# Optimization experiments

Hardware: AMD Instinct MI355X
Metric: run time of the kernel (lower is better)

## Reference

```python
import jax, jax.numpy as jnp
import numpy as np

IN_DIM = 512
OUT_DIM = 512


def setup_inputs() -> dict:
    key = jax.random.key(0)
    ks = jax.random.split(key, 7)
    B, S = 4, 2048
    scale = 1.0 / np.sqrt(IN_DIM)
    X = jax.random.normal(ks[0], (B, S, IN_DIM), dtype=jnp.float32)
    Wq = jax.random.normal(ks[1], (IN_DIM, OUT_DIM), dtype=jnp.float32) * scale
    Wk = jax.random.normal(ks[2], (IN_DIM, OUT_DIM), dtype=jnp.float32) * scale
    Wv = jax.random.normal(ks[3], (IN_DIM, OUT_DIM), dtype=jnp.float32) * scale
    bq = jnp.zeros((OUT_DIM,), dtype=jnp.float32)
    bk = jnp.zeros((OUT_DIM,), dtype=jnp.float32)
    bv = jnp.zeros((OUT_DIM,), dtype=jnp.float32)
    return {"X": X, "Wq": Wq, "bq": bq, "Wk": Wk, "bk": bk, "Wv": Wv, "bv": bv}


def reference(X, Wq, bq, Wk, bk, Wv, bv):
    # Q/K/V projections: [B,S,in] @ [in,out] -> [B,S,out]
    Q = X @ Wq + bq
    K = X @ Wk + bk
    V = X @ Wv + bv
    d_k = jnp.asarray(Q.shape[-1], Q.dtype)
    # scores: [B,S,S] = QK^T / sqrt(d_k)
    scores = jnp.einsum('bsd,btd->bst', Q, K) / jnp.sqrt(d_k)
    attn = jax.nn.softmax(scores, axis=-1)
    # out: [B,S,out]
    return jnp.einsum('bst,btd->bsd', attn, V)
```

## Files before the change

### kernel.cpp

```cpp
#include <hip/hip_runtime.h>
#include <hip/hip_bf16.h>
#include <stdint.h>

#define SEQ   2048
#define DIM   512
#define BATCH 4

typedef __attribute__((ext_vector_type(8))) short  short8;
typedef __attribute__((ext_vector_type(4))) float  floatx4;

static __device__ __forceinline__ unsigned short f2b(float f) {
  return __builtin_bit_cast(unsigned short, __float2bfloat16(f));
}

static __device__ __forceinline__ void gll16(const void* g, void* l) {
  __builtin_amdgcn_global_load_lds(
      (__attribute__((address_space(1))) void*)(uintptr_t)g,
      (__attribute__((address_space(3))) void*)l, 16, 0, 0);
}


template <int BF>
__device__ __forceinline__ void fgemm_lds(
    const char* __restrict__ A, int rtA0, int TKA,
    const char* __restrict__ B, int rtB0, int TKB,
    int kIters, char* lds, floatx4 (&acc)[4][BF / 2])
{
  constexpr int BUF = (8 + BF) * 1024;
  const int tid = threadIdx.x;
  const int w = tid >> 6, l = tid & 63;
  const int wmf = (w & 1) * 4;
  const int wnf = (w >> 1) * (BF / 2);

  auto stage = [&](int p, int kt) {
    char* dst = lds + p * BUF;
#pragma unroll
    for (int q = 0; q < 2; ++q) {
      const int f = q * 4 + w;
      gll16(A + (((size_t)(rtA0 + f) * TKA + kt) << 10) + l * 16,
            dst + f * 1024 + l * 16);
    }
#pragma unroll
    for (int q = 0; q < BF / 4; ++q) {
      const int f = q * 4 + w;
      gll16(B + (((size_t)(rtB0 + f) * TKB + kt) << 10) + l * 16,
            dst + 8192 + f * 1024 + l * 16);
    }
  };

  stage(0, 0);
  __syncthreads();

  for (int kt = 0; kt < kIters; ++kt) {
    const int p = kt & 1;
    if (kt + 1 < kIters) stage(1 - p, kt + 1);

    const char* bA = lds + p * BUF;
    const char* bB = bA + 8192;
    short8 af[4], bf[BF / 2];
#pragma unroll
    for (int i = 0; i < 4; ++i)
      af[i] = *(const short8*)(bA + (wmf + i) * 1024 + l * 16);
#pragma unroll
    for (int j = 0; j < BF / 2; ++j)
      bf[j] = *(const short8*)(bB + (wnf + j) * 1024 + l * 16);

#pragma unroll
    for (int i = 0; i < 4; ++i)
#pragma unroll
      for (int j = 0; j < BF / 2; ++j)
        acc[i][j] = __builtin_amdgcn_mfma_f32_16x16x32_bf16(af[i], bf[j], acc[i][j], 0, 0, 0);

    __syncthreads();
  }
}

__global__ __launch_bounds__(256) void setup_kernel(
    const float* __restrict__ X, const float* __restrict__ Wq,
    const float* __restrict__ Wk, const float* __restrict__ Wv,
    short8* __restrict__ XbF, short8* __restrict__ WF,
    float* __restrict__ rowsum)
{
  const int flat = blockIdx.x * 256 + threadIdx.x;
  {
    const int tile = flat >> 6, l = flat & 63;
    const int row = (tile >> 4) * 16 + (l & 15);
    const int k0  = (tile & 15) * 32 + (l >> 4) * 8;
    const float4 v0 = *(const float4*)(X + (size_t)row * DIM + k0);
    const float4 v1 = *(const float4*)(X + (size_t)row * DIM + k0 + 4);
    short8 o;
    o[0] = (short)f2b(v0.x); o[1] = (short)f2b(v0.y);
    o[2] = (short)f2b(v0.z); o[3] = (short)f2b(v0.w);
    o[4] = (short)f2b(v1.x); o[5] = (short)f2b(v1.y);
    o[6] = (short)f2b(v1.z); o[7] = (short)f2b(v1.w);
    XbF[flat] = o;
  }
  if (flat < 3 * 32768) {
    const int z = flat >> 15, within = flat & 32767;
    const float* W = (z == 0) ? Wq : (z == 1) ? Wk : Wv;
    const int tile = within >> 6, l = within & 63;
    const int n  = (tile >> 4) * 16 + (l & 15);
    const int k0 = (tile & 15) * 32 + (l >> 4) * 8;
    short8 o;
#pragma unroll
    for (int e = 0; e < 8; ++e)
      o[e] = (short)f2b(W[(size_t)(k0 + e) * DIM + n]);
    WF[flat] = o;
  }
  if (flat < 2048) ((float4*)rowsum)[flat] = float4{0.f, 0.f, 0.f, 0.f};
}

__global__ __launch_bounds__(256) void qkv_kernel(
    const short8* __restrict__ XbF, const short8* __restrict__ WF,
    const float* __restrict__ bq, const float* __restrict__ bk,
    const float* __restrict__ bv,
    unsigned short* __restrict__ QF, unsigned short* __restrict__ KF,
    unsigned short* __restrict__ VF)
{
  __shared__ char lds[32768];
  const int z = blockIdx.z, x = blockIdx.x, y = blockIdx.y;
  const int lane = threadIdx.x & 63, w = threadIdx.x >> 6;
  const char* Xc = (const char*)XbF;
  const char* Wc = (const char*)WF;
  floatx4 acc[4][4] = {};

  if (z < 2) {
    fgemm_lds<8>(Wc + (size_t)z * 524288, y * 8, 16, Xc, x * 8, 16, 16, lds, acc);
    const float* bias = z ? bk : bq;
    unsigned short* OF = z ? KF : QF;
    const int dbase = y * 128 + (w & 1) * 64;
    const int sbase = x * 128 + (w >> 1) * 64;
#pragma unroll
    for (int i = 0; i < 4; ++i) {
      const int d0 = dbase + i * 16 + (lane >> 4) * 4;
      const float4 b4 = *(const float4*)(bias + d0);
#pragma unroll
      for (int j = 0; j < 4; ++j) {
        const int s = sbase + j * 16 + (lane & 15);
        ushort4 pk;
        pk.x = f2b(acc[i][j][0] + b4.x);
        pk.y = f2b(acc[i][j][1] + b4.y);
        pk.z = f2b(acc[i][j][2] + b4.z);
        pk.w = f2b(acc[i][j][3] + b4.w);
        *(ushort4*)(OF + (size_t)((s >> 4) * 16 + (d0 >> 5)) * 512 +
                    ((((d0 & 31) >> 3) << 4) | (s & 15)) * 8 + (d0 & 7)) = pk;
      }
    }
  } else {
    fgemm_lds<8>(Xc, x * 8, 16, Wc + 2 * 524288, y * 8, 16, 16, lds, acc);
    const int sbase = x * 128 + (w & 1) * 64;
    const int dbase = y * 128 + (w >> 1) * 64;
#pragma unroll
    for (int i = 0; i < 4; ++i) {
      const int s0 = sbase + i * 16 + (lane >> 4) * 4;
      const int bt = s0 >> 11, t0 = s0 & 2047;
#pragma unroll
      for (int j = 0; j < 4; ++j) {
        const int d = dbase + j * 16 + (lane & 15);
        const float bn = bv[d];
        ushort4 pk;
        pk.x = f2b(acc[i][j][0] + bn);
        pk.y = f2b(acc[i][j][1] + bn);
        pk.z = f2b(acc[i][j][2] + bn);
        pk.w = f2b(acc[i][j][3] + bn);
        *(ushort4*)(VF + (size_t)bt * DIM * SEQ +
                    (size_t)((d >> 4) * 64 + (t0 >> 5)) * 512 +
                    ((((t0 & 31) >> 3) << 4) | (d & 15)) * 8 + (t0 & 7)) = pk;
      }
    }
  }
}

__global__ __launch_bounds__(256) void scores_kernel(
    const unsigned short* __restrict__ QF, const unsigned short* __restrict__ KF,
    unsigned short* __restrict__ ScF, float* __restrict__ rowsum)
{
  __shared__ char lds[32768];
  const int b = blockIdx.z, x = blockIdx.x, y = blockIdx.y;
  const int lane = threadIdx.x & 63, w = threadIdx.x >> 6;
  floatx4 acc[4][4] = {};
  fgemm_lds<8>((const char*)KF + (size_t)b * 2097152, y * 8, 16,
               (const char*)QF + (size_t)b * 2097152, x * 8, 16, 16, lds, acc);

  unsigned short* S = ScF + (size_t)b * SEQ * SEQ;
  const float scale = 0.044194173824159216f;
  const int tb = y * 128 + (w & 1) * 64;
  const int sb = x * 128 + (w >> 1) * 64;
  float colsum[4] = {0.f, 0.f, 0.f, 0.f};
#pragma unroll
  for (int i = 0; i < 4; ++i) {
    const int t0 = tb + i * 16 + (lane >> 4) * 4;
#pragma unroll
    for (int j = 0; j < 4; ++j) {
      const int s = sb + j * 16 + (lane & 15);
      float e0 = __expf(acc[i][j][0] * scale);
      float e1 = __expf(acc[i][j][1] * scale);
      float e2 = __expf(acc[i][j][2] * scale);
      float e3 = __expf(acc[i][j][3] * scale);
      colsum[j] += (e0 + e1) + (e2 + e3);
      ushort4 pk;
      pk.x = f2b(e0); pk.y = f2b(e1); pk.z = f2b(e2); pk.w = f2b(e3);
      *(ushort4*)(S + (size_t)((s >> 4) * 64 + (t0 >> 5)) * 512 +
                  ((((t0 & 31) >> 3) << 4) | (s & 15)) * 8 + (t0 & 7)) = pk;
    }
  }
#pragma unroll
  for (int j = 0; j < 4; ++j) {
    colsum[j] += __shfl_xor(colsum[j], 16, 64);
    colsum[j] += __shfl_xor(colsum[j], 32, 64);
  }
  if (lane < 16) {
#pragma unroll
    for (int j = 0; j < 4; ++j)
      atomicAdd(rowsum + b * SEQ + sb + j * 16 + lane, colsum[j]);
  }
}

__global__ __launch_bounds__(256) void pv_kernel(
    const unsigned short* __restrict__ ScF, const unsigned short* __restrict__ VF,
    const float* __restrict__ rowsum, float* __restrict__ out)
{
  __shared__ char lds[24576];
  const int b = blockIdx.z, x = blockIdx.x, y = blockIdx.y;
  const int lane = threadIdx.x & 63, w = threadIdx.x >> 6;
  floatx4 acc[4][2] = {};
  fgemm_lds<4>((const char*)ScF + (size_t)b * 8388608, x * 8, 64,
               (const char*)VF + (size_t)b * 2097152, y * 4, 64, 64, lds, acc);

#pragma unroll
  for (int i = 0; i < 4; ++i) {
    const int m0 = x * 128 + (w & 1) * 64 + i * 16 + (lane >> 4) * 4;
    const float4 rs = *(const float4*)(rowsum + b * SEQ + m0);
    const float inv0 = 1.f / rs.x, inv1 = 1.f / rs.y, inv2 = 1.f / rs.z, inv3 = 1.f / rs.w;
#pragma unroll
    for (int j = 0; j < 2; ++j) {
      const int d = y * 64 + (w >> 1) * 32 + j * 16 + (lane & 15);
      float* o = out + ((size_t)b * SEQ + m0) * DIM + d;
      o[0 * DIM] = acc[i][j][0] * inv0;
      o[1 * DIM] = acc[i][j][1] * inv1;
      o[2 * DIM] = acc[i][j][2] * inv2;
      o[3 * DIM] = acc[i][j][3] * inv3;
    }
  }
}

extern "C" void kernel_launch(void* const* d_in, const int* in_sizes, int n_in,
                              void* d_out, int out_size, void* d_ws, size_t ws_size,
                              hipStream_t stream) {
  const float* X  = (const float*)d_in[0];
  const float* Wq = (const float*)d_in[1];
  const float* bq = (const float*)d_in[2];
  const float* Wk = (const float*)d_in[3];
  const float* bk = (const float*)d_in[4];
  const float* Wv = (const float*)d_in[5];
  const float* bv = (const float*)d_in[6];
  float* out = (float*)d_out;
  char* ws = (char*)d_ws;

  short8* XbF = (short8*)(ws + 0);
  short8* WF  = (short8*)(ws + 8388608);
  char*   QF  = ws + 9961472;
  char*   KF  = ws + 18350080;
  char*   VF  = ws + 26738688;
  char*   ScF = ws + 35127296;
  float*  rowsum = (float*)(ws + 68681728);

  setup_kernel<<<dim3(2048), 256, 0, stream>>>(X, Wq, Wk, Wv, XbF, WF, rowsum);
  qkv_kernel<<<dim3(64, 4, 3), 256, 0, stream>>>(
      XbF, WF, bq, bk, bv,
      (unsigned short*)QF, (unsigned short*)KF, (unsigned short*)VF);
  scores_kernel<<<dim3(16, 16, 4), 256, 0, stream>>>(
      (const unsigned short*)QF, (const unsigned short*)KF,
      (unsigned short*)ScF, rowsum);
  pv_kernel<<<dim3(16, 8, 4), 256, 0, stream>>>(
      (const unsigned short*)ScF, (const unsigned short*)VF, rowsum, out);
}
```

Before: 150.4 us.

## Generalize LDS GEMM helper and enlarge block tiles to 512-thread blocks

The double-buffered LDS GEMM helper is made generic over A/B fragment counts, the warp grid shape and a K-chunk depth. With it, the QKV, scores and PV kernels move to 8-wave blocks with larger output tiles: 256x128 for QKV, 256x256 for scores, and 128x128 with two K-chunks per stage for PV. Grids shrink to match. Larger tiles raise operand reuse, cut redundant global and LDS staging traffic, and halve the barrier count in PV. The cost is fewer blocks (256 for scores and PV), more LDS per block and more accumulator registers, which can reduce occupancy and latency hiding.

```diff
diff --git a/kernel.cpp b/kernel.cpp
--- a/kernel.cpp
+++ b/kernel.cpp
@@ -20,31 +20,34 @@
 }
 
 
-template <int BF>
-__device__ __forceinline__ void fgemm_lds(
+template <int AF, int BF, int WM, int WN, int KC>
+__device__ __forceinline__ void fgemm8(
     const char* __restrict__ A, int rtA0, int TKA,
     const char* __restrict__ B, int rtB0, int TKB,
-    int kIters, char* lds, floatx4 (&acc)[4][BF / 2])
-{
-  constexpr int BUF = (8 + BF) * 1024;
+    int kIters, char* lds, floatx4 (&acc)[AF / WM][BF / WN])
+{
+  constexpr int AWF = AF / WM, BWF = BF / WN;
+  constexpr int BUF = (AF + BF) * KC * 1024;
   const int tid = threadIdx.x;
   const int w = tid >> 6, l = tid & 63;
-  const int wmf = (w & 1) * 4;
-  const int wnf = (w >> 1) * (BF / 2);
+  const int wm = w % WM, wn = w / WM;
 
   auto stage = [&](int p, int kt) {
     char* dst = lds + p * BUF;
 #pragma unroll
-    for (int q = 0; q < 2; ++q) {
-      const int f = q * 4 + w;
-      gll16(A + (((size_t)(rtA0 + f) * TKA + kt) << 10) + l * 16,
-            dst + f * 1024 + l * 16);
-    }
-#pragma unroll
-    for (int q = 0; q < BF / 4; ++q) {
-      const int f = q * 4 + w;
-      gll16(B + (((size_t)(rtB0 + f) * TKB + kt) << 10) + l * 16,
-            dst + 8192 + f * 1024 + l * 16);
+    for (int c = 0; c < KC; ++c) {
+#pragma unroll
+      for (int q = 0; q < AF / 8; ++q) {
+        const int f = q * 8 + w;
+        gll16(A + (((size_t)(rtA0 + f) * TKA + kt * KC + c) << 10) + l * 16,
+              dst + (c * AF + f) * 1024 + l * 16);
+      }
+#pragma unroll
+      for (int q = 0; q < BF / 8; ++q) {
+        const int f = q * 8 + w;
+        gll16(B + (((size_t)(rtB0 + f) * TKB + kt * KC + c) << 10) + l * 16,
+              dst + (KC * AF + c * BF + f) * 1024 + l * 16);
+      }
     }
   };
 
@@ -56,20 +59,24 @@
     if (kt + 1 < kIters) stage(1 - p, kt + 1);
 
     const char* bA = lds + p * BUF;
-    const char* bB = bA + 8192;
-    short8 af[4], bf[BF / 2];
-#pragma unroll
-    for (int i = 0; i < 4; ++i)
-      af[i] = *(const short8*)(bA + (wmf + i) * 1024 + l * 16);
-#pragma unroll
-    for (int j = 0; j < BF / 2; ++j)
-      bf[j] = *(const short8*)(bB + (wnf + j) * 1024 + l * 16);
-
-#pragma unroll
-    for (int i = 0; i < 4; ++i)
-#pragma unroll
-      for (int j = 0; j < BF / 2; ++j)
-        acc[i][j] = __builtin_amdgcn_mfma_f32_16x16x32_bf16(af[i], bf[j], acc[i][j], 0, 0, 0);
+    const char* bB = bA + KC * AF * 1024;
+    short8 af[KC][AWF], bf[KC][BWF];
+#pragma unroll
+    for (int c = 0; c < KC; ++c) {
+#pragma unroll
+      for (int i = 0; i < AWF; ++i)
+        af[c][i] = *(const short8*)(bA + (c * AF + wm * AWF + i) * 1024 + l * 16);
+#pragma unroll
+      for (int j = 0; j < BWF; ++j)
+        bf[c][j] = *(const short8*)(bB + (c * BF + wn * BWF + j) * 1024 + l * 16);
+    }
+#pragma unroll
+    for (int c = 0; c < KC; ++c)
+#pragma unroll
+      for (int i = 0; i < AWF; ++i)
+#pragma unroll
+        for (int j = 0; j < BWF; ++j)
+          acc[i][j] = __builtin_amdgcn_mfma_f32_16x16x32_bf16(af[c][i], bf[c][j], acc[i][j], 0, 0, 0);
 
     __syncthreads();
   }
@@ -110,26 +117,29 @@
   if (flat < 2048) ((float4*)rowsum)[flat] = float4{0.f, 0.f, 0.f, 0.f};
 }
 
-__global__ __launch_bounds__(256) void qkv_kernel(
+__global__ __launch_bounds__(512, 2) void qkv_kernel(
     const short8* __restrict__ XbF, const short8* __restrict__ WF,
     const float* __restrict__ bq, const float* __restrict__ bk,
     const float* __restrict__ bv,
     unsigned short* __restrict__ QF, unsigned short* __restrict__ KF,
     unsigned short* __restrict__ VF)
 {
-  __shared__ char lds[32768];
-  const int z = blockIdx.z, x = blockIdx.x, y = blockIdx.y;
+  __shared__ char lds[49152];
+  const int z = blockIdx.z, job = blockIdx.x;
   const int lane = threadIdx.x & 63, w = threadIdx.x >> 6;
+  const int wm = w & 3, wn = w >> 2;
   const char* Xc = (const char*)XbF;
   const char* Wc = (const char*)WF;
   floatx4 acc[4][4] = {};
 
   if (z < 2) {
-    fgemm_lds<8>(Wc + (size_t)z * 524288, y * 8, 16, Xc, x * 8, 16, 16, lds, acc);
+    const int x = job & 63, y = job >> 6;
+    fgemm8<16, 8, 4, 2, 1>(Wc + (size_t)z * 524288, y * 16, 16,
+                           Xc, x * 8, 16, 16, lds, acc);
     const float* bias = z ? bk : bq;
     unsigned short* OF = z ? KF : QF;
-    const int dbase = y * 128 + (w & 1) * 64;
-    const int sbase = x * 128 + (w >> 1) * 64;
+    const int dbase = y * 256 + wm * 64;
+    const int sbase = x * 128 + wn * 64;
 #pragma unroll
     for (int i = 0; i < 4; ++i) {
       const int d0 = dbase + i * 16 + (lane >> 4) * 4;
@@ -147,9 +157,11 @@
       }
     }
   } else {
-    fgemm_lds<8>(Xc, x * 8, 16, Wc + 2 * 524288, y * 8, 16, 16, lds, acc);
-    const int sbase = x * 128 + (w & 1) * 64;
-    const int dbase = y * 128 + (w >> 1) * 64;
+    const int x = job >> 2, y = job & 3;
+    fgemm8<16, 8, 4, 2, 1>(Xc, x * 16, 16,
+                           Wc + 2 * 524288, y * 8, 16, 16, lds, acc);
+    const int sbase = x * 256 + wm * 64;
+    const int dbase = y * 128 + wn * 64;
 #pragma unroll
     for (int i = 0; i < 4; ++i) {
       const int s0 = sbase + i * 16 + (lane >> 4) * 4;
@@ -171,28 +183,30 @@
   }
 }
 
-__global__ __launch_bounds__(256) void scores_kernel(
+__global__ __launch_bounds__(512, 2) void scores_kernel(
     const unsigned short* __restrict__ QF, const unsigned short* __restrict__ KF,
     unsigned short* __restrict__ ScF, float* __restrict__ rowsum)
 {
-  __shared__ char lds[32768];
+  __shared__ char lds[65536];
   const int b = blockIdx.z, x = blockIdx.x, y = blockIdx.y;
   const int lane = threadIdx.x & 63, w = threadIdx.x >> 6;
-  floatx4 acc[4][4] = {};
-  fgemm_lds<8>((const char*)KF + (size_t)b * 2097152, y * 8, 16,
-               (const char*)QF + (size_t)b * 2097152, x * 8, 16, 16, lds, acc);
+  const int wm = w & 1, wn = w >> 1;
+  floatx4 acc[8][4] = {};
+  fgemm8<16, 16, 2, 4, 1>((const char*)KF + (size_t)b * 2097152, y * 16, 16,
+                          (const char*)QF + (size_t)b * 2097152, x * 16, 16,
+                          16, lds, acc);
 
   unsigned short* S = ScF + (size_t)b * SEQ * SEQ;
   const float scale = 0.044194173824159216f;
-  const int tb = y * 128 + (w & 1) * 64;
-  const int sb = x * 128 + (w >> 1) * 64;
+  const int tbase = y * 256 + wm * 128;
+  const int sbase = x * 256 + wn * 64;
   float colsum[4] = {0.f, 0.f, 0.f, 0.f};
 #pragma unroll
-  for (int i = 0; i < 4; ++i) {
-    const int t0 = tb + i * 16 + (lane >> 4) * 4;
+  for (int i = 0; i < 8; ++i) {
+    const int t0 = tbase + i * 16 + (lane >> 4) * 4;
 #pragma unroll
     for (int j = 0; j < 4; ++j) {
-      const int s = sb + j * 16 + (lane & 15);
+      const int s = sbase + j * 16 + (lane & 15);
       float e0 = __expf(acc[i][j][0] * scale);
       float e1 = __expf(acc[i][j][1] * scale);
       float e2 = __expf(acc[i][j][2] * scale);
@@ -212,29 +226,33 @@
   if (lane < 16) {
 #pragma unroll
     for (int j = 0; j < 4; ++j)
-      atomicAdd(rowsum + b * SEQ + sb + j * 16 + lane, colsum[j]);
-  }
-}
-
-__global__ __launch_bounds__(256) void pv_kernel(
+      atomicAdd(rowsum + b * SEQ + sbase + j * 16 + lane, colsum[j]);
+  }
+}
+
+__global__ __launch_bounds__(512, 2) void pv_kernel(
     const unsigned short* __restrict__ ScF, const unsigned short* __restrict__ VF,
     const float* __restrict__ rowsum, float* __restrict__ out)
 {
-  __shared__ char lds[24576];
+  __shared__ char lds[65536];
   const int b = blockIdx.z, x = blockIdx.x, y = blockIdx.y;
   const int lane = threadIdx.x & 63, w = threadIdx.x >> 6;
+  const int wm = w & 1, wn = w >> 1;
   floatx4 acc[4][2] = {};
-  fgemm_lds<4>((const char*)ScF + (size_t)b * 8388608, x * 8, 64,
-               (const char*)VF + (size_t)b * 2097152, y * 4, 64, 64, lds, acc);
-
+  fgemm8<8, 8, 2, 4, 2>((const char*)ScF + (size_t)b * 8388608, x * 8, 64,
+                        (const char*)VF + (size_t)b * 2097152, y * 8, 64,
+                        32, lds, acc);
+
+  const int mbase = x * 128 + wm * 64;
+  const int dbase = y * 128 + wn * 32;
 #pragma unroll
   for (int i = 0; i < 4; ++i) {
-    const int m0 = x * 128 + (w & 1) * 64 + i * 16 + (lane >> 4) * 4;
+    const int m0 = mbase + i * 16 + (lane >> 4) * 4;
     const float4 rs = *(const float4*)(rowsum + b * SEQ + m0);
     const float inv0 = 1.f / rs.x, inv1 = 1.f / rs.y, inv2 = 1.f / rs.z, inv3 = 1.f / rs.w;
 #pragma unroll
     for (int j = 0; j < 2; ++j) {
-      const int d = y * 64 + (w >> 1) * 32 + j * 16 + (lane & 15);
+      const int d = dbase + j * 16 + (lane & 15);
       float* o = out + ((size_t)b * SEQ + m0) * DIM + d;
       o[0 * DIM] = acc[i][j][0] * inv0;
       o[1 * DIM] = acc[i][j][1] * inv1;
@@ -266,12 +284,12 @@
   float*  rowsum = (float*)(ws + 68681728);
 
   setup_kernel<<<dim3(2048), 256, 0, stream>>>(X, Wq, Wk, Wv, XbF, WF, rowsum);
-  qkv_kernel<<<dim3(64, 4, 3), 256, 0, stream>>>(
+  qkv_kernel<<<dim3(128, 1, 3), 512, 0, stream>>>(
       XbF, WF, bq, bk, bv,
       (unsigned short*)QF, (unsigned short*)KF, (unsigned short*)VF);
-  scores_kernel<<<dim3(16, 16, 4), 256, 0, stream>>>(
+  scores_kernel<<<dim3(8, 8, 4), 512, 0, stream>>>(
       (const unsigned short*)QF, (const unsigned short*)KF,
       (unsigned short*)ScF, rowsum);
-  pv_kernel<<<dim3(16, 8, 4), 256, 0, stream>>>(
+  pv_kernel<<<dim3(16, 4, 4), 512, 0, stream>>>(
       (const unsigned short*)ScF, (const unsigned short*)VF, rowsum, out);
 }
```

New measurement: 150.2 us. About the same (-0.1%).

## Switch scores and PV GEMMs to 32x32x16 MFMA with 32-row fragment layout

Applied to the files above, without the earlier changes.

Adds a GEMM helper built on the 32x32x16 bf16 MFMA instruction and reworks the fragment layouts of Q, K, V and the score matrix to 32-row tiles to match it. The scores and PV kernels now use this helper, and PV tiles grow from 128x64 to 128x128 (half as many blocks), so each score tile is reloaded fewer times. The goal is fewer LDS reads per FLOP and less redundant traffic on the large score matrix, at the cost of larger accumulators per wave and fewer blocks for occupancy.

```diff
diff --git a/kernel.cpp b/kernel.cpp
--- a/kernel.cpp
+++ b/kernel.cpp
@@ -6,8 +6,9 @@
 #define DIM   512
 #define BATCH 4
 
-typedef __attribute__((ext_vector_type(8))) short  short8;
-typedef __attribute__((ext_vector_type(4))) float  floatx4;
+typedef __attribute__((ext_vector_type(8)))  short  short8;
+typedef __attribute__((ext_vector_type(4)))  float  floatx4;
+typedef __attribute__((ext_vector_type(16))) float  floatx16;
 
 static __device__ __forceinline__ unsigned short f2b(float f) {
   return __builtin_bit_cast(unsigned short, __float2bfloat16(f));
@@ -70,6 +71,58 @@
 #pragma unroll
       for (int j = 0; j < BF / 2; ++j)
         acc[i][j] = __builtin_amdgcn_mfma_f32_16x16x32_bf16(af[i], bf[j], acc[i][j], 0, 0, 0);
+
+    __syncthreads();
+  }
+}
+
+template <int KC>
+__device__ __forceinline__ void fgemm32(
+    const char* __restrict__ A, int rtA0, int TKA,
+    const char* __restrict__ B, int rtB0, int TKB,
+    int kIters, char* lds, floatx16 (&acc)[2][2])
+{
+  constexpr int BUF = 8 * KC * 1024;
+  const int tid = threadIdx.x;
+  const int w = tid >> 6, l = tid & 63;
+  const int wm = w & 1, wn = w >> 1;
+
+  auto stage = [&](int p, int kt) {
+    char* dst = lds + p * BUF;
+#pragma unroll
+    for (int c = 0; c < KC; ++c) {
+      gll16(A + (((size_t)(rtA0 + w) * TKA + kt * KC + c) << 10) + l * 16,
+            dst + (c * 8 + w) * 1024 + l * 16);
+      gll16(B + (((size_t)(rtB0 + w) * TKB + kt * KC + c) << 10) + l * 16,
+            dst + (c * 8 + 4 + w) * 1024 + l * 16);
+    }
+  };
+
+  stage(0, 0);
+  __syncthreads();
+
+  for (int kt = 0; kt < kIters; ++kt) {
+    const int p = kt & 1;
+    if (kt + 1 < kIters) stage(1 - p, kt + 1);
+
+    const char* buf = lds + p * BUF;
+    short8 af[KC][2], bf[KC][2];
+#pragma unroll
+    for (int c = 0; c < KC; ++c) {
+#pragma unroll
+      for (int i = 0; i < 2; ++i)
+        af[c][i] = *(const short8*)(buf + (c * 8 + wm * 2 + i) * 1024 + l * 16);
+#pragma unroll
+      for (int j = 0; j < 2; ++j)
+        bf[c][j] = *(const short8*)(buf + (c * 8 + 4 + wn * 2 + j) * 1024 + l * 16);
+    }
+#pragma unroll
+    for (int c = 0; c < KC; ++c)
+#pragma unroll
+      for (int i = 0; i < 2; ++i)
+#pragma unroll
+        for (int j = 0; j < 2; ++j)
+          acc[i][j] = __builtin_amdgcn_mfma_f32_32x32x16_bf16(af[c][i], bf[c][j], acc[i][j], 0, 0, 0);
 
     __syncthreads();
   }
@@ -142,8 +195,8 @@
         pk.y = f2b(acc[i][j][1] + b4.y);
         pk.z = f2b(acc[i][j][2] + b4.z);
         pk.w = f2b(acc[i][j][3] + b4.w);
-        *(ushort4*)(OF + (size_t)((s >> 4) * 16 + (d0 >> 5)) * 512 +
-                    ((((d0 & 31) >> 3) << 4) | (s & 15)) * 8 + (d0 & 7)) = pk;
+        *(ushort4*)(OF + (size_t)((s >> 5) * 32 + (d0 >> 4)) * 512 +
+                    (((d0 >> 3) & 1) * 32 + (s & 31)) * 8 + (d0 & 7)) = pk;
       }
     }
   } else {
@@ -164,8 +217,8 @@
         pk.z = f2b(acc[i][j][2] + bn);
         pk.w = f2b(acc[i][j][3] + bn);
         *(ushort4*)(VF + (size_t)bt * DIM * SEQ +
-                    (size_t)((d >> 4) * 64 + (t0 >> 5)) * 512 +
-                    ((((t0 & 31) >> 3) << 4) | (d & 15)) * 8 + (t0 & 7)) = pk;
+                    (size_t)((d >> 5) * 128 + (t0 >> 4)) * 512 +
+                    (((t0 >> 3) & 1) * 32 + (d & 31)) * 8 + (t0 & 7)) = pk;
       }
     }
   }
@@ -178,41 +231,43 @@
   __shared__ char lds[32768];
   const int b = blockIdx.z, x = blockIdx.x, y = blockIdx.y;
   const int lane = threadIdx.x & 63, w = threadIdx.x >> 6;
-  floatx4 acc[4][4] = {};
-  fgemm_lds<8>((const char*)KF + (size_t)b * 2097152, y * 8, 16,
-               (const char*)QF + (size_t)b * 2097152, x * 8, 16, 16, lds, acc);
-
-  unsigned short* S = ScF + (size_t)b * SEQ * SEQ;
+  const int wm = w & 1, wn = w >> 1;
+  floatx16 acc[2][2] = {};
+  fgemm32<2>((const char*)KF + (size_t)b * 2097152, y * 4, 32,
+             (const char*)QF + (size_t)b * 2097152, x * 4, 32, 16, lds, acc);
+
+  unsigned short* S = ScF + (size_t)b * SEQ * SEQ / 1;
   const float scale = 0.044194173824159216f;
-  const int tb = y * 128 + (w & 1) * 64;
-  const int sb = x * 128 + (w >> 1) * 64;
-  float colsum[4] = {0.f, 0.f, 0.f, 0.f};
-#pragma unroll
-  for (int i = 0; i < 4; ++i) {
-    const int t0 = tb + i * 16 + (lane >> 4) * 4;
-#pragma unroll
-    for (int j = 0; j < 4; ++j) {
-      const int s = sb + j * 16 + (lane & 15);
-      float e0 = __expf(acc[i][j][0] * scale);
-      float e1 = __expf(acc[i][j][1] * scale);
-      float e2 = __expf(acc[i][j][2] * scale);
-      float e3 = __expf(acc[i][j][3] * scale);
-      colsum[j] += (e0 + e1) + (e2 + e3);
-      ushort4 pk;
-      pk.x = f2b(e0); pk.y = f2b(e1); pk.z = f2b(e2); pk.w = f2b(e3);
-      *(ushort4*)(S + (size_t)((s >> 4) * 64 + (t0 >> 5)) * 512 +
-                  ((((t0 & 31) >> 3) << 4) | (s & 15)) * 8 + (t0 & 7)) = pk;
-    }
-  }
-#pragma unroll
-  for (int j = 0; j < 4; ++j) {
-    colsum[j] += __shfl_xor(colsum[j], 16, 64);
-    colsum[j] += __shfl_xor(colsum[j], 32, 64);
-  }
-  if (lane < 16) {
-#pragma unroll
-    for (int j = 0; j < 4; ++j)
-      atomicAdd(rowsum + b * SEQ + sb + j * 16 + lane, colsum[j]);
+  const int tb = y * 128 + wm * 64;
+  const int sb = x * 128 + wn * 64;
+  float csum[2] = {0.f, 0.f};
+#pragma unroll
+  for (int i = 0; i < 2; ++i) {
+#pragma unroll
+    for (int j = 0; j < 2; ++j) {
+      const int s = sb + j * 32 + (lane & 31);
+      float e[16];
+#pragma unroll
+      for (int r = 0; r < 16; ++r) {
+        e[r] = __expf(acc[i][j][r] * scale);
+        csum[j] += e[r];
+      }
+#pragma unroll
+      for (int q = 0; q < 4; ++q) {
+        const int t = tb + i * 32 + (lane >> 5) * 4 + q * 8;
+        ushort4 pk;
+        pk.x = f2b(e[q * 4 + 0]); pk.y = f2b(e[q * 4 + 1]);
+        pk.z = f2b(e[q * 4 + 2]); pk.w = f2b(e[q * 4 + 3]);
+        *(ushort4*)(S + (size_t)((s >> 5) * 128 + (t >> 4)) * 512 +
+                    (((t >> 3) & 1) * 32 + (s & 31)) * 8 + (t & 7)) = pk;
+      }
+    }
+  }
+#pragma unroll
+  for (int j = 0; j < 2; ++j) {
+    csum[j] += __shfl_xor(csum[j], 32, 64);
+    if (lane < 32)
+      atomicAdd(rowsum + b * SEQ + sb + j * 32 + lane, csum[j]);
   }
 }
 
@@ -220,26 +275,29 @@
     const unsigned short* __restrict__ ScF, const unsigned short* __restrict__ VF,
     const float* __restrict__ rowsum, float* __restrict__ out)
 {
-  __shared__ char lds[24576];
+  __shared__ char lds[32768];
   const int b = blockIdx.z, x = blockIdx.x, y = blockIdx.y;
   const int lane = threadIdx.x & 63, w = threadIdx.x >> 6;
-  floatx4 acc[4][2] = {};
-  fgemm_lds<4>((const char*)ScF + (size_t)b * 8388608, x * 8, 64,
-               (const char*)VF + (size_t)b * 2097152, y * 4, 64, 64, lds, acc);
-
-#pragma unroll
-  for (int i = 0; i < 4; ++i) {
-    const int m0 = x * 128 + (w & 1) * 64 + i * 16 + (lane >> 4) * 4;
-    const float4 rs = *(const float4*)(rowsum + b * SEQ + m0);
-    const float inv0 = 1.f / rs.x, inv1 = 1.f / rs.y, inv2 = 1.f / rs.z, inv3 = 1.f / rs.w;
+  const int wm = w & 1, wn = w >> 1;
+  floatx16 acc[2][2] = {};
+  fgemm32<2>((const char*)ScF + (size_t)b * 8388608, x * 4, 128,
+             (const char*)VF + (size_t)b * 2097152, y * 4, 128, 64, lds, acc);
+
+#pragma unroll
+  for (int i = 0; i < 2; ++i) {
 #pragma unroll
     for (int j = 0; j < 2; ++j) {
-      const int d = y * 64 + (w >> 1) * 32 + j * 16 + (lane & 15);
-      float* o = out + ((size_t)b * SEQ + m0) * DIM + d;
-      o[0 * DIM] = acc[i][j][0] * inv0;
-      o[1 * DIM] = acc[i][j][1] * inv1;
-      o[2 * DIM] = acc[i][j][2] * inv2;
-      o[3 * DIM] = acc[i][j][3] * inv3;
+      const int d = y * 128 + wn * 64 + j * 32 + (lane & 31);
+#pragma unroll
+      for (int q = 0; q < 4; ++q) {
+        const int s0 = x * 128 + wm * 64 + i * 32 + (lane >> 5) * 4 + q * 8;
+        const float4 rs = *(const float4*)(rowsum + b * SEQ + s0);
+        float* o = out + ((size_t)b * SEQ + s0) * DIM + d;
+        o[0 * DIM] = acc[i][j][q * 4 + 0] * (1.f / rs.x);
+        o[1 * DIM] = acc[i][j][q * 4 + 1] * (1.f / rs.y);
+        o[2 * DIM] = acc[i][j][q * 4 + 2] * (1.f / rs.z);
+        o[3 * DIM] = acc[i][j][q * 4 + 3] * (1.f / rs.w);
+      }
     }
   }
 }
@@ -272,6 +330,6 @@
   scores_kernel<<<dim3(16, 16, 4), 256, 0, stream>>>(
       (const unsigned short*)QF, (const unsigned short*)KF,
       (unsigned short*)ScF, rowsum);
-  pv_kernel<<<dim3(16, 8, 4), 256, 0, stream>>>(
+  pv_kernel<<<dim3(16, 4, 4), 256, 0, stream>>>(
       (const unsigned short*)ScF, (const unsigned short*)VF, rowsum, out);
 }
```

After: 152.1 us. Within noise of the previous version (+1.2%).
